# Performance work log

Hardware: AMD Instinct MI355X
Metric: run time of the kernel (lower is better)

## Reference

```python
import jax, jax.numpy as jnp
import numpy as np


def setup_inputs() -> dict:
    key = jax.random.key(0)
    k1, k2, k3 = jax.random.split(key, 3)
    B, Cin, Cout, K, H, W = 4, 64, 64, 3, 160, 160
    inputs = jax.random.normal(k1, (B, Cin, H, W), dtype=jnp.float32)
    # fractional dilation rates in [1, 3]
    rate_map = 1.0 + 2.0 * jax.random.uniform(k2, (B, 1, H, W), dtype=jnp.float32)
    # xavier-uniform-ish init
    limit = float(np.sqrt(6.0 / (Cin * K * K + Cout * K * K)))
    weight = jax.random.uniform(k3, (Cout, Cin, K, K), dtype=jnp.float32,
                                minval=-limit, maxval=limit)
    bias = jnp.zeros((Cout,), dtype=jnp.float32)
    return {"inputs": inputs, "weight": weight, "rate_map": rate_map,
            "bias": bias, "stride_h": 1, "stride_w": 1}


def _pdconv2d(inputs, weight, rate_map, bias, stride_h, stride_w):
    """Perspective (fractional, per-pixel) dilated conv with same padding.

    For each output pixel, the KxK taps are placed at center + offset*rate,
    where rate comes from rate_map and may be fractional -> bilinear sampling
    with zeros outside the image.
    """
    B, C, H, W = inputs.shape
    O, _, K, _ = weight.shape
    HO = (H + stride_h - 1) // stride_h
    WO = (W + stride_w - 1) // stride_w

    rate = rate_map[:, 0, ::stride_h, ::stride_w]  # [B,HO,WO]
    cy = (jnp.arange(HO) * stride_h).astype(jnp.float32)
    cx = (jnp.arange(WO) * stride_w).astype(jnp.float32)
    off = jnp.arange(K, dtype=jnp.float32) - (K - 1) / 2.0  # centered taps

    # sampling coords [B,HO,WO,K,K]
    sy = cy[None, :, None, None, None] + off[None, None, None, :, None] * rate[:, :, :, None, None]
    sx = cx[None, None, :, None, None] + off[None, None, None, None, :] * rate[:, :, :, None, None]
    sy = jnp.broadcast_to(sy, (B, HO, WO, K, K))
    sx = jnpp = jnp.broadcast_to(sx, (B, HO, WO, K, K))
    sx = jnp_p = sx  # no-op alias (keeps names clear)

    y0 = jnp.floor(sy)
    x0 = jnp.floor(sx)
    wy = sy - y0  # bilinear weights
    wx = sx - x0
    y0i = y0.astype(jnp.int32)
    x0i = x0.astype(jnp.int32)

    img = inputs.reshape(B, C, H * W)

    def gather(idx):  # idx [B,HO,WO,K,K] -> [B,C,HO,WO,K,K]
        return jax.vmap(lambda im, ix: jnp.take(im, ix, axis=-1))(img, idx)

    acc = jnp.zeros((B, C, HO, WO, K, K), dtype=inputs.dtype)
    corners = [(0, 0, (1 - wy) * (1 - wx)), (0, 1, (1 - wy) * wx),
               (1, 0, wy * (1 - wx)), (1, 1, wy * wx)]
    for dy, dx, cw in corners:
        yy = y0i + dy
        xx = x0i + dx
        valid = (yy >= 0) & (yy < H) & (xx >= 0) & (xx < W)
        idx = jnp.clip(yy, 0, H - 1) * W + jnp.clip(xx, 0, W - 1)
        w = (cw * valid.astype(inputs.dtype))[:, None]  # [B,1,HO,WO,K,K]
        acc = acc + gather(idx) * w

    # [B,C,HO,WO,K,K] x [O,C,K,K] -> [B,O,HO,WO]
    out = jnp.einsum('bchwkl,ockl->bohw', acc, weight)
    return out + bias[None, :, None, None]


def reference(inputs, weight, rate_map, bias, stride_h, stride_w):
    return _pdconv2d(inputs, weight, rate_map, bias, stride_h, stride_w)
```

## Files before the change

kernel.cpp:

```cpp
#include <hip/hip_runtime.h>
#include <hip/hip_bf16.h>

#define NB   4
#define CIN  64
#define COUT 64
#define HH   160
#define WW   160
#define HW   (HH * WW)

#define RT   9
#define CT   39
#define RS   72
#define HIN_SHORTS (RT * CT * RS)

typedef __attribute__((ext_vector_type(8))) short bf16x8;
typedef __attribute__((ext_vector_type(4))) float f32x4;
typedef __attribute__((ext_vector_type(2))) float f32x2;
typedef __attribute__((ext_vector_type(4))) unsigned int u32x4;

static __device__ __forceinline__ short f2bf(float v) {
    return __builtin_bit_cast(short, __float2bfloat16(v));
}

__global__ void wtf_kernel(const float* __restrict__ w, short* __restrict__ wtf) {
    int i = blockIdx.x * 256 + threadIdx.x;
    if (i < 36864) {
        const int j  = i & 7;
        const int l  = (i >> 3) & 63;
        const int mt = (i >> 9) & 3;
        const int ks = (i >> 11) & 1;
        const int t  = i >> 12;
        const int o  = 16 * mt + (l & 15);
        const int c  = 32 * ks + 8 * (l >> 4) + j;
        wtf[i] = f2bf(w[(o * CIN + c) * 9 + t]);
    }
}

__global__ __launch_bounds__(256) void tin_kernel(const float* __restrict__ in,
                                                  short* __restrict__ tin) {
    const int cpx = gridDim.x >> 3;
    const int wb  = (blockIdx.x & 7) * cpx + (blockIdx.x >> 3);
    const int gid = wb * 256 + threadIdx.x;
    if (gid >= NB * HW) return;
    const int b  = gid / HW;
    const int hw = gid - b * HW;
    const float* src = in + (size_t)b * CIN * HW + hw;
    short* dst = tin + (size_t)gid * CIN;
#pragma unroll
    for (int chunk = 0; chunk < 4; ++chunk) {
        union { u32x4 v; short s[8]; } p0, p1;
#pragma unroll
        for (int cc = 0; cc < 8; ++cc)
            p0.s[cc] = f2bf(src[(size_t)(chunk * 16 + cc) * HW]);
#pragma unroll
        for (int cc = 0; cc < 8; ++cc)
            p1.s[cc] = f2bf(src[(size_t)(chunk * 16 + 8 + cc) * HW]);
        *(u32x4*)(dst + chunk * 16)     = p0.v;
        *(u32x4*)(dst + chunk * 16 + 8) = p1.v;
    }
}

static __device__ __forceinline__ void consume_tap(
    const u32x4 v00, const u32x4 v01, const u32x4 v10, const u32x4 v11,
    const float c00, const float c01, const float c10, const float c11,
    const bf16x8 wf0, const bf16x8 wf1, const bf16x8 wf2, const bf16x8 wf3,
    f32x4 acc[4])
{
    union { bf16x8 v; unsigned u[4]; } pf;
#pragma unroll
    for (int wd = 0; wd < 4; ++wd) {
        f32x2 s;
        {
            const unsigned u0 = v00[wd];
            const f32x2 xv = { __builtin_bit_cast(float, u0 << 16),
                               __builtin_bit_cast(float, u0 & 0xffff0000u) };
            s = c00 * xv;
        }
        {
            const unsigned u0 = v01[wd];
            const f32x2 xv = { __builtin_bit_cast(float, u0 << 16),
                               __builtin_bit_cast(float, u0 & 0xffff0000u) };
            s += c01 * xv;
        }
        {
            const unsigned u0 = v10[wd];
            const f32x2 xv = { __builtin_bit_cast(float, u0 << 16),
                               __builtin_bit_cast(float, u0 & 0xffff0000u) };
            s += c10 * xv;
        }
        {
            const unsigned u0 = v11[wd];
            const f32x2 xv = { __builtin_bit_cast(float, u0 << 16),
                               __builtin_bit_cast(float, u0 & 0xffff0000u) };
            s += c11 * xv;
        }
        unsigned r;
        asm("v_cvt_pk_bf16_f32 %0, %1, %2" : "=v"(r) : "v"(s.x), "v"(s.y));
        pf.u[wd] = r;
    }
    acc[0] = __builtin_amdgcn_mfma_f32_16x16x32_bf16(wf0, pf.v, acc[0], 0, 0, 0);
    acc[1] = __builtin_amdgcn_mfma_f32_16x16x32_bf16(wf1, pf.v, acc[1], 0, 0, 0);
    acc[2] = __builtin_amdgcn_mfma_f32_16x16x32_bf16(wf2, pf.v, acc[2], 0, 0, 0);
    acc[3] = __builtin_amdgcn_mfma_f32_16x16x32_bf16(wf3, pf.v, acc[3], 0, 0, 0);
}

__global__ __launch_bounds__(256, 3) void pdconv_halo_kernel(
    const short* __restrict__ tin,
    const short* __restrict__ wtf,
    const float* __restrict__ rate_map,
    const float* __restrict__ bias,
    float* __restrict__ out)
{
    __shared__ short hin[HIN_SHORTS];

    const int tid  = threadIdx.x;
    const int wave = tid >> 6;
    const int lane = tid & 63;
    const int px   = lane & 15;
    const int g    = lane >> 4;

    const int cpx = gridDim.x >> 3;
    const int bid = (blockIdx.x & 7) * cpx + (blockIdx.x >> 3);

    const int b   = bid / 400;
    const int rem = bid - b * 400;
    const int rr  = rem / 5;
    const int cc  = rem - rr * 5;
    const int oy  = 2 * rr - 3;
    const int ox  = 32 * cc - 3;

    const short* ib = tin + (size_t)b * HW * CIN;
#pragma unroll
    for (int it = 0; it < 11; ++it) {
        const int idx = it * 256 + tid;
        if (idx < RT * CT * 8) {
            const int rec = idx >> 3;
            const int cp  = idx & 7;
            const int ty  = rec / CT;
            const int tx  = rec - ty * CT;
            const int gy  = min(max(oy + ty, 0), HH - 1);
            const int gx  = min(max(ox + tx, 0), WW - 1);
            const u32x4 v = *(const u32x4*)(ib + ((size_t)gy * WW + gx) * CIN + cp * 8);
            *(u32x4*)(hin + rec * RS + cp * 8) = v;
        }
    }

    const int row  = 2 * rr + (wave >> 1);
    const int col0 = 32 * cc + 16 * (wave & 1);
    const int x    = col0 + px;
    const float rate = rate_map[b * HW + row * WW + x];
    const float fy = (float)row, fx = (float)x;

    const short* wtb = wtf + lane * 8;

    f32x4 acc[4];
#pragma unroll
    for (int mt = 0; mt < 4; ++mt) acc[mt] = (f32x4){0.f, 0.f, 0.f, 0.f};

    u32x4 vi00[2][2], vi01[2][2], vi10[2][2], vi11[2][2];
    float cf[2][4];

#define GEOMH(T, SL, H0) do {                                                \
    const int gky = (T) / 3, gkx = (T) - 3 * gky;                            \
    const float gsy = fy + (float)(gky - 1) * rate;                          \
    const float gsx = fx + (float)(gkx - 1) * rate;                          \
    const float gy0f = floorf(gsy), gx0f = floorf(gsx);                      \
    const float gwy = gsy - gy0f, gwx = gsx - gx0f;                          \
    const int gy0 = (int)gy0f, gx0 = (int)gx0f;                              \
    const float gomwy = 1.0f - gwy, gomwx = 1.0f - gwx;                      \
    const float gvy0 = (gy0 >= 0 && gy0 < HH) ? 1.0f : 0.0f;                 \
    const float gvy1 = (gy0 + 1 >= 0 && gy0 + 1 < HH) ? 1.0f : 0.0f;         \
    const float gvx0 = (gx0 >= 0 && gx0 < WW) ? 1.0f : 0.0f;                 \
    const float gvx1 = (gx0 + 1 >= 0 && gx0 + 1 < WW) ? 1.0f : 0.0f;         \
    cf[SL][0] = gomwy * gomwx * gvy0 * gvx0;                                 \
    cf[SL][1] = gomwy * gwx   * gvy0 * gvx1;                                 \
    cf[SL][2] = gwy   * gomwx * gvy1 * gvx0;                                 \
    cf[SL][3] = gwy   * gwx   * gvy1 * gvx1;                                 \
    H0 = hin + ((gy0 - oy) * CT + (gx0 - ox)) * RS + 8 * g;                  \
} while (0)

#define LOADIN(T, SL) do {                                                   \
    const short* h00;                                                        \
    GEOMH(T, SL, h00);                                                       \
    _Pragma("unroll")                                                        \
    for (int ks = 0; ks < 2; ++ks) {                                         \
        const short* hk = h00 + 32 * ks;                                     \
        vi00[SL][ks] = *(const u32x4*)(hk);                                  \
        vi01[SL][ks] = *(const u32x4*)(hk + RS);                             \
        vi10[SL][ks] = *(const u32x4*)(hk + CT * RS);                        \
        vi11[SL][ks] = *(const u32x4*)(hk + (CT + 1) * RS);                  \
    }                                                                        \
} while (0)

    __syncthreads();
    LOADIN(0, 0);

#pragma unroll
    for (int t = 0; t < 9; ++t) {
        const int s = t & 1;
        if (t < 8) LOADIN(t + 1, (t + 1) & 1);
#pragma unroll
        for (int ks = 0; ks < 2; ++ks) {
            const short* wb = wtb + (size_t)((t * 2 + ks) * 4) * 512;
            const bf16x8 wf0 = *(const bf16x8*)(wb);
            const bf16x8 wf1 = *(const bf16x8*)(wb + 512);
            const bf16x8 wf2 = *(const bf16x8*)(wb + 1024);
            const bf16x8 wf3 = *(const bf16x8*)(wb + 1536);
            consume_tap(vi00[s][ks], vi01[s][ks], vi10[s][ks], vi11[s][ks],
                        cf[s][0], cf[s][1], cf[s][2], cf[s][3],
                        wf0, wf1, wf2, wf3, acc);
        }
    }
#undef LOADIN
#undef GEOMH

    float* op = out + (size_t)b * COUT * HW + row * WW + col0 + px;
#pragma unroll
    for (int mt = 0; mt < 4; ++mt) {
        const f32x4 bv = *(const f32x4*)(bias + 16 * mt + 4 * g);
#pragma unroll
        for (int r = 0; r < 4; ++r) {
            const int o = 16 * mt + 4 * g + r;
            op[(size_t)o * HW] = acc[mt][r] + bv[r];
        }
    }
}

__global__ void wt2_kernel(const float* __restrict__ w, short* __restrict__ wt2) {
    int i = blockIdx.x * 256 + threadIdx.x;
    if (i < 9 * COUT * CIN) {
        int c = i & 63, o = (i >> 6) & 63, t = i >> 12;
        wt2[i] = f2bf(w[(o * CIN + c) * 9 + t]);
    }
}

__global__ __launch_bounds__(256) void pdconv_mfma_kernel(
    const float* __restrict__ in, const short* __restrict__ wt2,
    const float* __restrict__ rate_map, const float* __restrict__ bias,
    float* __restrict__ out)
{
    const int tid = threadIdx.x, wave = tid >> 6, lane = tid & 63;
    const int px = lane & 15, g = lane >> 4;
    const int cpx = gridDim.x >> 3;
    const int bid = (blockIdx.x & 7) * cpx + (blockIdx.x >> 3);
    const int base = bid * 64 + wave * 16;
    const int b = base / HW, pix0 = base - b * HW;
    const int y = pix0 / WW, x0 = pix0 - y * WW, x = x0 + px;
    const float rate = rate_map[base + px];
    const float fy = (float)y, fx = (float)x;
    f32x4 acc[4];
#pragma unroll
    for (int mt = 0; mt < 4; ++mt) acc[mt] = (f32x4){0.f, 0.f, 0.f, 0.f};
    const float* img  = in + (size_t)b * CIN * HW;
    const float* imgg = img + (size_t)g * 8 * HW;
#pragma unroll 1
    for (int t = 0; t < 9; ++t) {
        const int ky = t / 3, kx = t - 3 * ky;
        const float sy = fy + (float)(ky - 1) * rate;
        const float sx = fx + (float)(kx - 1) * rate;
        const float y0f = floorf(sy), x0f = floorf(sx);
        const float wy = sy - y0f, wx = sx - x0f;
        const int y0 = (int)y0f, x0i = (int)x0f, y1 = y0 + 1, x1 = x0i + 1;
        const float omwy = 1.0f - wy, omwx = 1.0f - wx;
        const float vy0 = (y0 >= 0 && y0 < HH) ? 1.0f : 0.0f;
        const float vy1 = (y1 >= 0 && y1 < HH) ? 1.0f : 0.0f;
        const float vx0 = (x0i >= 0 && x0i < WW) ? 1.0f : 0.0f;
        const float vx1 = (x1 >= 0 && x1 < WW) ? 1.0f : 0.0f;
        const float c00 = omwy * omwx * vy0 * vx0, c01 = omwy * wx * vy0 * vx1;
        const float c10 = wy * omwx * vy1 * vx0,  c11 = wy * wx * vy1 * vx1;
        const int cy0 = min(max(y0, 0), HH - 1), cy1 = min(max(y1, 0), HH - 1);
        const int cx0 = min(max(x0i, 0), WW - 1), cx1 = min(max(x1, 0), WW - 1);
        const int i00 = cy0 * WW + cx0, i01 = cy0 * WW + cx1;
        const int i10 = cy1 * WW + cx0, i11 = cy1 * WW + cx1;
#pragma unroll
        for (int ks = 0; ks < 2; ++ks) {
            bf16x8 wf[4];
#pragma unroll
            for (int mt = 0; mt < 4; ++mt)
                wf[mt] = *(const bf16x8*)(wt2 +
                          ((t * COUT + 16 * mt + px) * CIN + 32 * ks + 8 * g));
            float a[8];
#pragma unroll
            for (int j = 0; j < 8; ++j) {
                const float* ch = imgg + (size_t)(32 * ks + j) * HW;
                a[j] = c00 * ch[i00] + c01 * ch[i01] + c10 * ch[i10] + c11 * ch[i11];
            }
            union { bf16x8 v; short s[8]; } pf;
#pragma unroll
            for (int j = 0; j < 8; ++j) pf.s[j] = f2bf(a[j]);
#pragma unroll
            for (int mt = 0; mt < 4; ++mt)
                acc[mt] = __builtin_amdgcn_mfma_f32_16x16x32_bf16(
                              wf[mt], pf.v, acc[mt], 0, 0, 0);
        }
    }
    float* op = out + (size_t)b * COUT * HW + pix0 + px;
#pragma unroll
    for (int mt = 0; mt < 4; ++mt)
#pragma unroll
        for (int r = 0; r < 4; ++r) {
            const int o = 16 * mt + 4 * g + r;
            op[(size_t)o * HW] = acc[mt][r] + bias[o];
        }
}

extern "C" void kernel_launch(void* const* d_in, const int* in_sizes, int n_in,
                              void* d_out, int out_size, void* d_ws, size_t ws_size,
                              hipStream_t stream) {
    (void)in_sizes; (void)n_in; (void)out_size;
    const float* in   = (const float*)d_in[0];
    const float* w    = (const float*)d_in[1];
    const float* rm   = (const float*)d_in[2];
    const float* bias = (const float*)d_in[3];
    float* out = (float*)d_out;

    const size_t WTF_BYTES = 36864 * sizeof(short);
    const size_t TIN_BYTES = (size_t)NB * HW * CIN * sizeof(short);

    if (ws_size >= WTF_BYTES + TIN_BYTES) {
        short* wtf = (short*)d_ws;
        short* tin = (short*)((char*)d_ws + WTF_BYTES);
        hipLaunchKernelGGL(wtf_kernel, dim3(144), dim3(256), 0, stream, w, wtf);
        hipLaunchKernelGGL(tin_kernel, dim3((NB * HW) / 256), dim3(256),
                           0, stream, in, tin);
        const int nblocks = NB * 80 * 5;
        hipLaunchKernelGGL(pdconv_halo_kernel, dim3(nblocks), dim3(256), 0,
                           stream, tin, wtf, rm, bias, out);
    } else {
        short* wt2 = (short*)d_ws;
        hipLaunchKernelGGL(wt2_kernel, dim3(144), dim3(256), 0, stream, w, wt2);
        hipLaunchKernelGGL(pdconv_mfma_kernel, dim3((NB * HW) / 64), dim3(256),
                           0, stream, in, wt2, rm, bias, out);
    }
}
```

Before: 46.78 us.

## Split input channels across wave pairs with LDS reduction, shrink tiles

Each block now covers a 2x16 output tile instead of 2x32, so the grid doubles. The two waves in a pair each handle half of the input channels for the same pixels, and their partial accumulators are summed through a shared-memory reduction buffer before the store. The halo tile shrinks to 8x22, launch bounds move to 4 blocks per CU, and the software double-buffering of tap loads is removed. Together these aim for more parallelism and occupancy, at the cost of a larger halo-to-interior ratio, an extra barrier and reduction step, and half the waves sitting idle during the store.

```diff
diff --git a/kernel.cpp b/kernel.cpp
--- a/kernel.cpp
+++ b/kernel.cpp
@@ -8,8 +8,8 @@
 #define WW   160
 #define HW   (HH * WW)
 
-#define RT   9
-#define CT   39
+#define RT   8
+#define CT   22
 #define RS   72
 #define HIN_SHORTS (RT * CT * RS)
 
@@ -104,7 +104,7 @@
     acc[3] = __builtin_amdgcn_mfma_f32_16x16x32_bf16(wf3, pf.v, acc[3], 0, 0, 0);
 }
 
-__global__ __launch_bounds__(256, 3) void pdconv_halo_kernel(
+__global__ __launch_bounds__(256, 4) void pdconv_tile_kernel(
     const short* __restrict__ tin,
     const short* __restrict__ wtf,
     const float* __restrict__ rate_map,
@@ -112,26 +112,29 @@
     float* __restrict__ out)
 {
     __shared__ short hin[HIN_SHORTS];
+    __shared__ float red[2][64][17];
 
     const int tid  = threadIdx.x;
     const int wave = tid >> 6;
     const int lane = tid & 63;
     const int px   = lane & 15;
     const int g    = lane >> 4;
+    const int r    = wave >> 1;
+    const int th   = wave & 1;
 
     const int cpx = gridDim.x >> 3;
     const int bid = (blockIdx.x & 7) * cpx + (blockIdx.x >> 3);
 
-    const int b   = bid / 400;
-    const int rem = bid - b * 400;
-    const int rr  = rem / 5;
-    const int cc  = rem - rr * 5;
+    const int b   = bid / 800;
+    const int rem = bid - b * 800;
+    const int rr  = rem / 10;
+    const int cc  = rem - rr * 10;
     const int oy  = 2 * rr - 3;
-    const int ox  = 32 * cc - 3;
+    const int ox  = 16 * cc - 3;
 
     const short* ib = tin + (size_t)b * HW * CIN;
 #pragma unroll
-    for (int it = 0; it < 11; ++it) {
+    for (int it = 0; it < 6; ++it) {
         const int idx = it * 256 + tid;
         if (idx < RT * CT * 8) {
             const int rec = idx >> 3;
@@ -145,9 +148,8 @@
         }
     }
 
-    const int row  = 2 * rr + (wave >> 1);
-    const int col0 = 32 * cc + 16 * (wave & 1);
-    const int x    = col0 + px;
+    const int row = 2 * rr + r;
+    const int x   = 16 * cc + px;
     const float rate = rate_map[b * HW + row * WW + x];
     const float fy = (float)row, fx = (float)x;
 
@@ -157,10 +159,9 @@
 #pragma unroll
     for (int mt = 0; mt < 4; ++mt) acc[mt] = (f32x4){0.f, 0.f, 0.f, 0.f};
 
-    u32x4 vi00[2][2], vi01[2][2], vi10[2][2], vi11[2][2];
-    float cf[2][4];
-
-#define GEOMH(T, SL, H0) do {                                                \
+    __syncthreads();
+
+#define DO_TAP(T) do {                                                       \
     const int gky = (T) / 3, gkx = (T) - 3 * gky;                            \
     const float gsy = fy + (float)(gky - 1) * rate;                          \
     const float gsx = fx + (float)(gkx - 1) * rate;                          \
@@ -172,56 +173,48 @@
     const float gvy1 = (gy0 + 1 >= 0 && gy0 + 1 < HH) ? 1.0f : 0.0f;         \
     const float gvx0 = (gx0 >= 0 && gx0 < WW) ? 1.0f : 0.0f;                 \
     const float gvx1 = (gx0 + 1 >= 0 && gx0 + 1 < WW) ? 1.0f : 0.0f;         \
-    cf[SL][0] = gomwy * gomwx * gvy0 * gvx0;                                 \
-    cf[SL][1] = gomwy * gwx   * gvy0 * gvx1;                                 \
-    cf[SL][2] = gwy   * gomwx * gvy1 * gvx0;                                 \
-    cf[SL][3] = gwy   * gwx   * gvy1 * gvx1;                                 \
-    H0 = hin + ((gy0 - oy) * CT + (gx0 - ox)) * RS + 8 * g;                  \
+    const float c00 = gomwy * gomwx * gvy0 * gvx0;                           \
+    const float c01 = gomwy * gwx   * gvy0 * gvx1;                           \
+    const float c10 = gwy   * gomwx * gvy1 * gvx0;                           \
+    const float c11 = gwy   * gwx   * gvy1 * gvx1;                           \
+    const short* hk = hin + ((gy0 - oy) * CT + (gx0 - ox)) * RS              \
+                          + 32 * th + 8 * g;                                 \
+    const u32x4 v00 = *(const u32x4*)(hk);                                   \
+    const u32x4 v01 = *(const u32x4*)(hk + RS);                              \
+    const u32x4 v10 = *(const u32x4*)(hk + CT * RS);                         \
+    const u32x4 v11 = *(const u32x4*)(hk + (CT + 1) * RS);                   \
+    const short* wb = wtb + (size_t)(((T) * 2 + th) * 4) * 512;              \
+    const bf16x8 wf0 = *(const bf16x8*)(wb);                                 \
+    const bf16x8 wf1 = *(const bf16x8*)(wb + 512);                           \
+    const bf16x8 wf2 = *(const bf16x8*)(wb + 1024);                          \
+    const bf16x8 wf3 = *(const bf16x8*)(wb + 1536);                          \
+    consume_tap(v00, v01, v10, v11, c00, c01, c10, c11,                      \
+                wf0, wf1, wf2, wf3, acc);                                    \
 } while (0)
 
-#define LOADIN(T, SL) do {                                                   \
-    const short* h00;                                                        \
-    GEOMH(T, SL, h00);                                                       \
-    _Pragma("unroll")                                                        \
-    for (int ks = 0; ks < 2; ++ks) {                                         \
-        const short* hk = h00 + 32 * ks;                                     \
-        vi00[SL][ks] = *(const u32x4*)(hk);                                  \
-        vi01[SL][ks] = *(const u32x4*)(hk + RS);                             \
-        vi10[SL][ks] = *(const u32x4*)(hk + CT * RS);                        \
-        vi11[SL][ks] = *(const u32x4*)(hk + (CT + 1) * RS);                  \
-    }                                                                        \
-} while (0)
-
+    DO_TAP(0); DO_TAP(1); DO_TAP(2); DO_TAP(3); DO_TAP(4);
+    DO_TAP(5); DO_TAP(6); DO_TAP(7); DO_TAP(8);
+#undef DO_TAP
+
+    if (th == 1) {
+#pragma unroll
+        for (int mt = 0; mt < 4; ++mt)
+#pragma unroll
+            for (int j = 0; j < 4; ++j)
+                red[r][lane][4 * mt + j] = acc[mt][j];
+    }
     __syncthreads();
-    LOADIN(0, 0);
-
-#pragma unroll
-    for (int t = 0; t < 9; ++t) {
-        const int s = t & 1;
-        if (t < 8) LOADIN(t + 1, (t + 1) & 1);
-#pragma unroll
-        for (int ks = 0; ks < 2; ++ks) {
-            const short* wb = wtb + (size_t)((t * 2 + ks) * 4) * 512;
-            const bf16x8 wf0 = *(const bf16x8*)(wb);
-            const bf16x8 wf1 = *(const bf16x8*)(wb + 512);
-            const bf16x8 wf2 = *(const bf16x8*)(wb + 1024);
-            const bf16x8 wf3 = *(const bf16x8*)(wb + 1536);
-            consume_tap(vi00[s][ks], vi01[s][ks], vi10[s][ks], vi11[s][ks],
-                        cf[s][0], cf[s][1], cf[s][2], cf[s][3],
-                        wf0, wf1, wf2, wf3, acc);
-        }
-    }
-#undef LOADIN
-#undef GEOMH
-
-    float* op = out + (size_t)b * COUT * HW + row * WW + col0 + px;
-#pragma unroll
-    for (int mt = 0; mt < 4; ++mt) {
-        const f32x4 bv = *(const f32x4*)(bias + 16 * mt + 4 * g);
-#pragma unroll
-        for (int r = 0; r < 4; ++r) {
-            const int o = 16 * mt + 4 * g + r;
-            op[(size_t)o * HW] = acc[mt][r] + bv[r];
+    if (th == 0) {
+        float* op = out + (size_t)b * COUT * HW + row * WW + 16 * cc + px;
+#pragma unroll
+        for (int mt = 0; mt < 4; ++mt) {
+            const f32x4 bv = *(const f32x4*)(bias + 16 * mt + 4 * g);
+#pragma unroll
+            for (int j = 0; j < 4; ++j) {
+                const int o = 16 * mt + 4 * g + j;
+                op[(size_t)o * HW] = acc[mt][j] + red[r][lane][4 * mt + j]
+                                   + bv[j];
+            }
         }
     }
 }
@@ -323,8 +316,8 @@
         hipLaunchKernelGGL(wtf_kernel, dim3(144), dim3(256), 0, stream, w, wtf);
         hipLaunchKernelGGL(tin_kernel, dim3((NB * HW) / 256), dim3(256),
                            0, stream, in, tin);
-        const int nblocks = NB * 80 * 5;
-        hipLaunchKernelGGL(pdconv_halo_kernel, dim3(nblocks), dim3(256), 0,
+        const int nblocks = NB * 80 * 10;
+        hipLaunchKernelGGL(pdconv_tile_kernel, dim3(nblocks), dim3(256), 0,
                            stream, tin, wtf, rm, bias, out);
     } else {
         short* wt2 = (short*)d_ws;
```

New measurement: 46.91 us. No clear change (+0.3%).
